# Optimization experiments

Measured on AMD Instinct MI355X. Metric: run time of the kernel, lower is better.

## Reference

```python
import jax, jax.numpy as jnp
import numpy as np
from jax import lax

V, E, H, B, P, Q = 50000, 300, 256, 32, 400, 40


def _cell(x, h, c, Wih, Whh, b):
    # torch nn.LSTMCell math (b = b_ih + b_hh), gate order i,f,g,o
    g = x @ Wih.T + h @ Whh.T + b
    i, f, gg, o = jnp.split(g, 4, axis=-1)
    c2 = jax.nn.sigmoid(f) * c + jax.nn.sigmoid(i) * jnp.tanh(gg)
    return jax.nn.sigmoid(o) * jnp.tanh(c2), c2


def setup_inputs():
    key = jax.random.key(0)
    ks = jax.random.split(key, 26)
    n = lambda k, s: jax.random.normal(k, s, jnp.float32) * 0.05
    return {
        "passage_ids": jax.random.randint(ks[0], (P, B), 0, V),
        "question_ids": jax.random.randint(ks[1], (Q, B), 0, V),
        "passage_lens": jax.random.randint(ks[2], (B,), P // 2, P + 1),
        "question_lens": jax.random.randint(ks[3], (B,), Q // 2, Q + 1),
        "answer": jax.random.randint(ks[4], (2, B), 0, P // 2),
        "embed": n(ks[5], (V, E)),
        "pre_Wih": n(ks[6], (4 * H, E)),
        "pre_Whh": n(ks[7], (4 * H, H)),
        "pre_b": n(ks[8], (4 * H,)),
        "Wq": n(ks[9], (H, H)),
        "Wp": n(ks[10], (H, H)),
        "bp": n(ks[11], (H,)),
        "Wh": n(ks[12], (H, H)),
        "w_alpha": n(ks[13], (H,)),
        "b_alpha": n(ks[14], ()),
        "m_Wih": n(ks[15], (4 * H, 2 * H)),
        "m_Whh": n(ks[16], (4 * H, H)),
        "m_b": n(ks[17], (4 * H,)),
        "Wm": n(ks[18], (2 * H, H)),
        "Wa": n(ks[19], (H, H)),
        "ba": n(ks[20], (H,)),
        "w_beta": n(ks[21], (H,)),
        "b_beta": n(ks[22], ()),
        "p_Wih": n(ks[23], (4 * H, 2 * H)),
        "p_Whh": n(ks[24], (4 * H, H)),
        "p_b": n(ks[25], (4 * H,)),
    }


def _forward(embed, pre_Wih, pre_Whh, pre_b, Wq, Wp, bp, Wh, w_alpha, b_alpha,
             m_Wih, m_Whh, m_b, Wm, Wa, ba, w_beta, b_beta, p_Wih, p_Whh, p_b,
             passage_ids, passage_lens, question_ids, question_lens):
    Hd = pre_Whh.shape[1]
    Bd = passage_ids.shape[1]
    z0 = jnp.zeros((Bd, Hd), jnp.float32)

    def preprocess(ids, lens):
        x = embed[ids]                                       # [T,B,E]
        T = x.shape[0]
        m = (jnp.arange(T)[:, None] < lens[None, :]).astype(jnp.float32)[:, :, None]  # [T,B,1]
        def step(carry, inp):
            h, c = carry
            xt, mt = inp
            _, c2 = _cell(xt, h, c, pre_Wih, pre_Whh, pre_b)
            h2 = jnp.tanh(c2) * mt                           # module quirk: h := tanh(c)
            return (h2, c2 * mt), h2
        _, Hs = lax.scan(step, (z0, z0), (x, m))
        return Hs, m

    Hp, mP = preprocess(passage_ids, passage_lens)           # [P,B,H]
    Hq, _ = preprocess(question_ids, question_lens)          # [Q,B,H]

    attQ = Hq @ Wq                                           # [Q,B,H]

    def match(Hp_dir, m_dir):
        def step(carry, inp):
            h, c = carry
            hp, mt = inp                                     # hp [B,H], mt [B,1]
            g = jnp.tanh(attQ + hp @ Wp + bp + h @ Wh)       # [Q,B,H]
            alpha = jax.nn.softmax(g @ w_alpha + b_alpha, axis=0)  # softmax over question time [Q,B]
            wq = jnp.einsum('qb,qbh->bh', alpha, Hq)
            zt = jnp.concatenate([hp, wq], axis=-1) * mt
            h2, c2 = _cell(zt, h, c, m_Wih, m_Whh, m_b)
            h2 = h2 * mt
            return (h2, c2 * mt), h2
        _, Hs = lax.scan(step, (z0, z0), (Hp_dir, m_dir))
        return Hs

    Hf = match(Hp, mP)
    Hb = match(Hp[::-1], mP[::-1])[::-1]
    Hr = jnp.concatenate([Hf, Hb], axis=-1)                  # [P,B,2H]

    attM = Hr @ Wm                                           # [P,B,H]
    valid = (jnp.arange(Hr.shape[0])[:, None] < passage_lens[None, :]).astype(jnp.float32)  # [P,B]
    ha, ca = z0, z0
    dists = []
    for _ in range(2):                                       # start / end pointer
        Fk = jnp.tanh(attM + ha @ Wa + ba)                   # [P,B,H]
        scores = Fk @ w_beta + b_beta                        # [P,B]
        scores = jnp.where(valid > 0, scores, -1e30)
        beta = jax.nn.softmax(scores, axis=0) * valid        # zeros past passage length, like original
        dists.append(beta.T)                                 # [B,P]
        wHr = jnp.einsum('pb,pbh->bh', beta, Hr)
        ha, ca = _cell(wHr, ha, ca, p_Wih, p_Whh, p_b)
    return jnp.stack(dists)                                  # [2,B,P]


def reference(passage_ids, question_ids, passage_lens, question_lens, answer,
              embed, pre_Wih, pre_Whh, pre_b, Wq, Wp, bp, Wh, w_alpha, b_alpha,
              m_Wih, m_Whh, m_b, Wm, Wa, ba, w_beta, b_beta, p_Wih, p_Whh, p_b):
    # `answer` only feeds the training loss in the original; forward returns the distributions.
    return _forward(embed, pre_Wih, pre_Whh, pre_b, Wq, Wp, bp, Wh, w_alpha, b_alpha,
                    m_Wih, m_Whh, m_b, Wm, Wa, ba, w_beta, b_beta, p_Wih, p_Whh, p_b,
                    passage_ids, passage_lens, question_ids, question_lens)
```

## Files before the change

### kernel.cpp

```cpp
#include <hip/hip_runtime.h>
#include <hip/hip_bf16.h>

typedef __attribute__((ext_vector_type(8))) short short8;
typedef __attribute__((ext_vector_type(4))) float f32x4;
typedef __attribute__((ext_vector_type(2))) float f32x2;
typedef unsigned short u16;
typedef unsigned int u32;

#define DEV __device__ __forceinline__

static constexpr int Hd    = 256;
static constexpr int Bb    = 32;
static constexpr int Pp    = 400;
static constexpr int Qq    = 40;
static constexpr int NROWS = Pp * Bb + Qq * Bb;
static constexpr int PROBE_MAGIC = 1234567;
static constexpr int NPROBE = 14;

DEV float bf2f(u16 u) { u32 i = ((u32)u) << 16; float f; __builtin_memcpy(&f, &i, 4); return f; }
DEV u16 f2bf(float f) { u32 i; __builtin_memcpy(&i, &f, 4); i += 0x7FFFu + ((i >> 16) & 1u); return (u16)(i >> 16); }
DEV float sigf(float x) { return __builtin_amdgcn_rcpf(1.f + __expf(-x)); }
DEV float tanhf_(float x) {
  float ax = __builtin_fabsf(x);
  float t = __expf(2.f * ax);
  float r = 1.f - 2.f * __builtin_amdgcn_rcpf(t + 1.f);
  return x < 0.f ? -r : r;
}
DEV f32x4 mfma32(short8 a, short8 b, f32x4 c) {
  return __builtin_amdgcn_mfma_f32_16x16x32_bf16(a, b, c, 0, 0, 0);
}
DEV short8 zero8() { short8 z = {0,0,0,0,0,0,0,0}; return z; }

struct KArgs {
  const int *pids, *qids, *plen, *qlen;
  const float *embedF, *preWihF, *preWhhF, *preBF, *WqF, *WpF, *bpF, *WhF,
              *walphaF, *balphaF, *mWihF, *mWhhF, *mBF, *WmF, *WaF, *baF,
              *wbetaF, *bbetaF, *pWihF, *pWhhF, *pBF;
  int* bar;
  u16 *WqT, *WpT, *WmT, *WihP, *Xpad, *preX, *Hp, *Hq, *Hrb, *wq, *wHr, *haB,
      *attQb, *pWihB, *pWhhB, *mWxb, *WhTb, *xW;
  float *hpWp, *attM, *scores, *aWa, *gatesW;
  float* out;
};

DEV void probe_mark(int* bar, int idx) {
  if (blockIdx.x == 0 && threadIdx.x == 0)
    __hip_atomic_store(bar + 768 + idx, PROBE_MAGIC, __ATOMIC_RELEASE, __HIP_MEMORY_SCOPE_AGENT);
}

DEV void barn(int* base, int grp, int n, int gen) {
  __syncthreads();
  if (threadIdx.x == 0) {
    int* c = base + grp * 128;
    int* g = base + grp * 128 + 64;
    if (__hip_atomic_fetch_add(c, 1, __ATOMIC_ACQ_REL, __HIP_MEMORY_SCOPE_AGENT) == n - 1) {
      __hip_atomic_store(c, 0, __ATOMIC_RELAXED, __HIP_MEMORY_SCOPE_AGENT);
      __hip_atomic_store(g, gen, __ATOMIC_RELEASE, __HIP_MEMORY_SCOPE_AGENT);
    } else {
      while (__hip_atomic_load(g, __ATOMIC_RELAXED, __HIP_MEMORY_SCOPE_AGENT) < gen)
        __builtin_amdgcn_s_sleep(1);
      __builtin_amdgcn_fence(__ATOMIC_ACQUIRE, "agent");
    }
  }
  __syncthreads();
}

__global__ __launch_bounds__(256) void k_prep(KArgs A) {
  const int gtid = blockIdx.x * 256 + threadIdx.x;
  const int GS = 256 * 256;
  for (int idx = gtid; idx < 1024 * 160; idx += GS) {
    int row = idx / 160, cd = idx - row * 160;
    u32 v = 0;
    if (cd < 150) {
      f32x2 e2 = *(const f32x2*)(A.preWihF + (size_t)row * 300 + cd * 2);
      v = (u32)f2bf(e2[0]) | ((u32)f2bf(e2[1]) << 16);
    }
    *(u32*)(A.WihP + (size_t)row * 320 + cd * 2) = v;
  }
  for (int idx = gtid; idx < NROWS * 160; idx += GS) {
    int row = idx / 160, cd = idx - row * 160;
    int id = (row < Pp * Bb) ? A.pids[row] : A.qids[row - Pp * Bb];
    u32 v = 0;
    if (cd < 150) {
      f32x2 e2 = *(const f32x2*)(A.embedF + (size_t)id * 300 + cd * 2);
      v = (u32)f2bf(e2[0]) | ((u32)f2bf(e2[1]) << 16);
    }
    *(u32*)(A.Xpad + (size_t)row * 320 + cd * 2) = v;
  }
  for (int idx = gtid; idx < 65536; idx += GS) {
    int r = idx >> 8, c = idx & 255;
    A.WqT[idx]  = f2bf(A.WqF[c * 256 + r]);
    A.WpT[idx]  = f2bf(A.WpF[c * 256 + r]);
    A.WhTb[idx] = f2bf(A.WhF[c * 256 + r]);
  }
  for (int idx = gtid; idx < 131072; idx += GS) {
    int r = idx >> 9, c = idx & 511;
    A.WmT[idx] = f2bf(A.WmF[c * 256 + r]);
  }
  for (int idx = gtid; idx < 1024 * 256; idx += GS) {
    int n = idx >> 8, k = idx & 255;
    A.mWxb[idx] = f2bf(A.mWihF[(size_t)n * 512 + k]);
  }
  for (int idx = gtid; idx < 524288 + 262144; idx += GS) {
    if (idx < 524288) A.pWihB[idx] = f2bf(A.pWihF[idx]);
    else              A.pWhhB[idx - 524288] = f2bf(A.pWhhF[idx - 524288]);
  }
  if (gtid < 32 * 256) {
    A.aWa[gtid] = A.baF[gtid & 255];
    A.haB[gtid] = 0;
  }
  probe_mark(A.bar, 0);
}

struct GemmArgs { const u16* Ag; int lda; const u16* Bg; int ldb; int Mt64, Nt64, nk; float* Cf; u16* Cb; int ldc; int* bar; int probe; };

__global__ __launch_bounds__(512) void k_gemm(GemmArgs g) {
  const int tid = threadIdx.x, lane = tid & 63;
  const int r16 = lane & 15, kl = (lane >> 4) * 8;
  const int ntile = g.Mt64 * g.Nt64;
  const int stride = gridDim.x * 8;
  for (int tix = blockIdx.x * 8 + (tid >> 6); tix < ntile; tix += stride) {
    int m0 = (tix / g.Nt64) * 64, n0 = (tix % g.Nt64) * 64;
    f32x4 acc[4][4] = {};
    for (int kb = 0; kb < g.nk; ++kb) {
      int k0 = kb * 32 + kl;
      short8 a[4], b[4];
#pragma unroll
      for (int i = 0; i < 4; ++i) {
        a[i] = *(const short8*)(g.Ag + (size_t)(m0 + i * 16 + r16) * g.lda + k0);
        b[i] = *(const short8*)(g.Bg + (size_t)(n0 + i * 16 + r16) * g.ldb + k0);
      }
#pragma unroll
      for (int mi = 0; mi < 4; ++mi)
#pragma unroll
        for (int ni = 0; ni < 4; ++ni) acc[mi][ni] = mfma32(a[mi], b[ni], acc[mi][ni]);
    }
#pragma unroll
    for (int mi = 0; mi < 4; ++mi)
#pragma unroll
      for (int ni = 0; ni < 4; ++ni)
#pragma unroll
        for (int j = 0; j < 4; ++j) {
          int r = m0 + mi * 16 + (lane >> 4) * 4 + j, cc = n0 + ni * 16 + r16;
          if (g.Cf) g.Cf[(size_t)r * g.ldc + cc] = acc[mi][ni][j];
          else      g.Cb[(size_t)r * g.ldc + cc] = f2bf(acc[mi][ni][j]);
        }
  }
  probe_mark(g.bar, g.probe);
}

__global__ __launch_bounds__(512) void k_prescan(KArgs A) {
  __shared__ __align__(16) unsigned char sm[33280];
  float* PRE = (float*)(sm + 24576);
  float* CL  = (float*)(sm + 30720);
  float* PBL = (float*)(sm + 32768);
  const int blk = blockIdx.x;
  const int gi  = blk & 15;
  const int grp = blk >> 4;
  const int steps  = grp ? Qq : Pp;
  const int* lens  = grp ? A.qlen : A.plen;
  u16* Hs          = grp ? A.Hq : A.Hp;
  const int xoff   = grp ? Pp * Bb : 0;

  const int tid = threadIdx.x, lane = tid & 63, wv = tid >> 6;
  const int r16 = lane & 15, kl = (lane >> 4) * 8;
  const int h0 = gi * 16;

  for (int idx = tid; idx < 48 * 256; idx += 512) {
    int row = idx >> 8, k = idx & 255;
    int gate = (row >> 4) * 256 + h0 + (row & 15);
    int byte = row * 512 + ((2 * k) ^ ((row & 7) << 4));
    *(u16*)(sm + byte) = f2bf(A.preWhhF[(size_t)gate * 256 + k]);
  }
  for (int idx = tid; idx < 32 * 16; idx += 512) CL[idx] = 0.f;
  if (tid < 48) PBL[tid] = A.preBF[(tid >> 4) * 256 + h0 + (tid & 15)];
  __syncthreads();

  int gen = 0;
#pragma unroll 1
  for (int t = 0; t < steps; ++t) {
    if (wv < 6) {
      int mi = wv & 1, ni = wv >> 1;
      int chain = mi * 16 + r16;
      f32x4 acc = {0.f, 0.f, 0.f, 0.f};
#pragma unroll
      for (int kb = 0; kb < 8; ++kb) {
        int k0 = kb * 32 + kl;
        short8 a = zero8();
        if (t > 0) a = *(const short8*)(Hs + (size_t)((t - 1) * 32 + chain) * 256 + k0);
        int row = ni * 16 + r16;
        short8 b = *(const short8*)(sm + row * 512 + ((2 * k0) ^ ((row & 7) << 4)));
        acc = mfma32(a, b, acc);
      }
      int col = ni * 16 + r16;
#pragma unroll
      for (int j = 0; j < 4; ++j)
        PRE[(mi * 16 + (lane >> 4) * 4 + j) * 48 + col] = acc[j];
    }
    __syncthreads();
    {
      int chain = tid >> 4, hd = tid & 15;
      size_t xr = (size_t)(xoff + t * 32 + chain) * 1024;
      float ip = PRE[chain * 48 + hd]      + bf2f(A.preX[xr + h0 + hd])       + PBL[hd];
      float fp = PRE[chain * 48 + 16 + hd] + bf2f(A.preX[xr + 256 + h0 + hd]) + PBL[16 + hd];
      float gp = PRE[chain * 48 + 32 + hd] + bf2f(A.preX[xr + 512 + h0 + hd]) + PBL[32 + hd];
      float c2 = sigf(fp) * CL[chain * 16 + hd] + sigf(ip) * tanhf_(gp);
      float mt = (t < lens[chain]) ? 1.f : 0.f;
      float h2 = tanhf_(c2) * mt;
      c2 *= mt;
      CL[chain * 16 + hd] = c2;
      Hs[(size_t)(t * 32 + chain) * 256 + h0 + hd] = f2bf(h2);
    }
    barn(A.bar, grp, 16, ++gen);
  }
  probe_mark(A.bar, 2);
}

__global__ __launch_bounds__(512) void k_match(KArgs A) {
  __shared__ __align__(16) unsigned char sm[81920];
  float* PRE = (float*)(sm + 65536);
  float* CL  = (float*)(sm + 73728);
  float* EL  = (float*)(sm + 75776);
  float* SL  = (float*)(sm + 77824);
  float* AL  = (float*)(sm + 78336);
  float* BPL = (float*)(sm + 78848);
  float* WAL = (float*)(sm + 79872);
  float* MBL = (float*)(sm + 80896);

  const int blk = blockIdx.x;
  const int gi  = blk & 15;
  const int dir = blk >> 4;
  const int grp = 2 + dir;
  const int tid = threadIdx.x, lane = tid & 63, wv = tid >> 6;
  const int r16 = lane & 15, kl = (lane >> 4) * 8;
  const int h0 = gi * 16;

  for (int idx = tid; idx < 64 * 512; idx += 512) {
    int row = idx >> 9, k = idx & 511;
    int gate = (row >> 4) * 256 + h0 + (row & 15);
    float v = (k < 256) ? A.mWihF[(size_t)gate * 512 + 256 + k]
                        : A.mWhhF[(size_t)gate * 256 + (k - 256)];
    int byte = row * 1024 + ((2 * k) ^ ((row & 7) << 4));
    *(u16*)(sm + byte) = f2bf(v);
  }
  for (int idx = tid; idx < 32 * 16; idx += 512) CL[idx] = 0.f;
  if (tid < 256) { BPL[tid] = A.bpF[tid]; WAL[tid] = A.walphaF[tid]; }
  if (tid < 64) MBL[tid] = A.mBF[(tid >> 4) * 256 + h0 + (tid & 15)];
  __syncthreads();

  const float bAl = A.balphaF[0];
  int gen = 0;
#pragma unroll 1
  for (int t = 0; t < Pp; ++t) {
    int p  = dir ? (Pp - 1 - t) : t;
    int pp = dir ? (p + 1) : (p - 1);
    barn(A.bar, grp, 16, ++gen);

    if (t == 0) {
      EL[tid] = 0.f;
    } else {
      f32x4 acc0 = {0.f,0.f,0.f,0.f}, acc1 = {0.f,0.f,0.f,0.f};
#pragma unroll
      for (int kb = 0; kb < 8; ++kb) {
        int k0 = kb * 32 + kl;
        short8 a = zero8();
        if (r16 < 2)
          a = *(const short8*)(A.Hrb + (size_t)(pp * 32 + gi * 2 + r16) * 512 + dir * 256 + k0);
        short8 bA = *(const short8*)(A.WhTb + (size_t)(wv * 32 + r16) * 256 + k0);
        short8 bB = *(const short8*)(A.WhTb + (size_t)(wv * 32 + 16 + r16) * 256 + k0);
        acc0 = mfma32(a, bA, acc0);
        acc1 = mfma32(a, bB, acc1);
      }
      if ((lane >> 4) == 0) {
        EL[0 * 256 + wv * 32 + r16]      = acc0[0];
        EL[1 * 256 + wv * 32 + r16]      = acc0[1];
        EL[0 * 256 + wv * 32 + 16 + r16] = acc1[0];
        EL[1 * 256 + wv * 32 + 16 + r16] = acc1[1];
      }
    }
    __syncthreads();
    {
      int c = wv >> 2;
      int b = gi * 2 + c;
      float base[4];
#pragma unroll
      for (int j = 0; j < 4; ++j) {
        int h = lane + 64 * j;
        base[j] = A.hpWp[(size_t)(p * 32 + b) * 256 + h] + BPL[h] + EL[c * 256 + h];
      }
      int q4 = wv & 3;
#pragma unroll
      for (int i = 0; i < 10; ++i) {
        int q = q4 + 4 * i;
        float s = 0.f;
#pragma unroll
        for (int j = 0; j < 4; ++j) {
          int h = lane + 64 * j;
          s += WAL[h] * tanhf_(bf2f(A.attQb[(size_t)(q * 32 + b) * 256 + h]) + base[j]);
        }
#pragma unroll
        for (int off = 32; off; off >>= 1) s += __shfl_xor(s, off, 64);
        if (lane == 0) SL[c * 40 + q] = s;
      }
    }
    __syncthreads();
    if ((wv & 3) == 0) {
      int c = wv >> 2;
      float x = (lane < 40) ? (SL[c * 40 + lane] + bAl) : -3.4e38f;
      float m = x;
#pragma unroll
      for (int off = 32; off; off >>= 1) m = fmaxf(m, __shfl_xor(m, off, 64));
      float e = (lane < 40) ? __expf(x - m) : 0.f;
      float su = e;
#pragma unroll
      for (int off = 32; off; off >>= 1) su += __shfl_xor(su, off, 64);
      if (lane < 40) AL[c * 40 + lane] = e / su;
    }
    __syncthreads();
    {
      int c = tid >> 8, h = tid & 255;
      int b = gi * 2 + c;
      float acc = 0.f;
#pragma unroll 8
      for (int q = 0; q < 40; ++q) acc += AL[c * 40 + q] * bf2f(A.Hq[(size_t)(q * 32 + b) * 256 + h]);
      float mt = (p < A.plen[b]) ? 1.f : 0.f;
      A.wq[(size_t)(dir * 32 + b) * 256 + h] = f2bf(acc * mt);
    }
    barn(A.bar, grp, 16, ++gen);

    {
      int mi = wv >> 2, ni = wv & 3;
      int chain = mi * 16 + r16;
      f32x4 acc = {0.f, 0.f, 0.f, 0.f};
#pragma unroll
      for (int kb = 0; kb < 16; ++kb) {
        int k0 = kb * 32 + kl;
        short8 a;
        if (kb < 8) a = *(const short8*)(A.wq + (size_t)(dir * 32 + chain) * 256 + k0);
        else {
          if (t == 0) a = zero8();
          else        a = *(const short8*)(A.Hrb + (size_t)(pp * 32 + chain) * 512 + dir * 256 + (k0 - 256));
        }
        int row = ni * 16 + r16;
        short8 b = *(const short8*)(sm + row * 1024 + ((2 * k0) ^ ((row & 7) << 4)));
        acc = mfma32(a, b, acc);
      }
      int col = ni * 16 + r16;
#pragma unroll
      for (int j = 0; j < 4; ++j)
        PRE[(mi * 16 + (lane >> 4) * 4 + j) * 64 + col] = acc[j];
    }
    __syncthreads();
    {
      int chain = tid >> 4, hd = tid & 15;
      size_t xr = (size_t)(p * 32 + chain) * 1024 + h0 + hd;
      float ig = PRE[chain * 64 + hd]      + MBL[hd]      + bf2f(A.xW[xr]);
      float fg = PRE[chain * 64 + 16 + hd] + MBL[16 + hd] + bf2f(A.xW[xr + 256]);
      float gg = PRE[chain * 64 + 32 + hd] + MBL[32 + hd] + bf2f(A.xW[xr + 512]);
      float og = PRE[chain * 64 + 48 + hd] + MBL[48 + hd] + bf2f(A.xW[xr + 768]);
      float c2 = sigf(fg) * CL[chain * 16 + hd] + sigf(ig) * tanhf_(gg);
      float h2 = sigf(og) * tanhf_(c2);
      float mt = (p < A.plen[chain]) ? 1.f : 0.f;
      c2 *= mt; h2 *= mt;
      CL[chain * 16 + hd] = c2;
      A.Hrb[(size_t)(p * 32 + chain) * 512 + dir * 256 + h0 + hd] = f2bf(h2);
    }
  }
  probe_mark(A.bar, 6);
}

__global__ __launch_bounds__(512) void k_scores(KArgs A, int probe) {
  const int blk = blockIdx.x, tid = threadIdx.x, lane = tid & 63, wv = tid >> 6;
  for (int j = wv; j < 50; j += 8) {
    int id = blk * 50 + j;
    int p = id >> 5, b = id & 31;
    float s = 0.f;
#pragma unroll
    for (int jj = 0; jj < 4; ++jj) {
      int h = lane + 64 * jj;
      s += A.wbetaF[h] * tanhf_(A.attM[(size_t)(p * 32 + b) * 256 + h] + A.aWa[b * 256 + h]);
    }
#pragma unroll
    for (int off = 32; off; off >>= 1) s += __shfl_xor(s, off, 64);
    if (lane == 0)
      A.scores[p * 32 + b] = (p < A.plen[b]) ? (s + A.bbetaF[0]) : -1e30f;
  }
  probe_mark(A.bar, probe);
}

__global__ __launch_bounds__(512) void k_soft(KArgs A, int k, int probe) {
  __shared__ __align__(16) unsigned char sm[2048];
  float* BL = (float*)sm;
  float* RED = (float*)(sm + 1664);
  const int b = blockIdx.x, tid = threadIdx.x, lane = tid & 63, wv = tid >> 6;
  float x = (tid < 400) ? A.scores[tid * 32 + b] : -3.4e38f;
  float m = x;
#pragma unroll
  for (int off = 32; off; off >>= 1) m = fmaxf(m, __shfl_xor(m, off, 64));
  if (lane == 0) RED[wv] = m;
  __syncthreads();
  if (tid == 0) {
    float mm = RED[0];
#pragma unroll
    for (int i = 1; i < 8; ++i) mm = fmaxf(mm, RED[i]);
    RED[0] = mm;
  }
  __syncthreads();
  float M = RED[0];
  float e = (tid < 400) ? __expf(x - M) : 0.f;
  float su = e;
#pragma unroll
  for (int off = 32; off; off >>= 1) su += __shfl_xor(su, off, 64);
  if (lane == 0) RED[8 + wv] = su;
  __syncthreads();
  if (tid == 0) {
    float ss = 0.f;
#pragma unroll
    for (int i = 0; i < 8; ++i) ss += RED[8 + i];
    RED[8] = ss;
  }
  __syncthreads();
  float SUM = RED[8];
  if (tid < 400) {
    float beta = (e / SUM) * ((tid < A.plen[b]) ? 1.f : 0.f);
    A.out[(size_t)(k * 32 + b) * 400 + tid] = beta;
    BL[tid] = beta;
  }
  if (k == 0) {
    __syncthreads();
    float acc = 0.f;
#pragma unroll 4
    for (int p = 0; p < 400; ++p) acc += BL[p] * bf2f(A.Hrb[(size_t)(p * 32 + b) * 512 + tid]);
    A.wHr[b * 512 + tid] = f2bf(acc);
  }
  probe_mark(A.bar, probe);
}

__global__ __launch_bounds__(128) void k_pgates(KArgs A) {
  const int blk = blockIdx.x, tid = threadIdx.x, lane = tid & 63, wv = tid >> 6;
  const int r16 = lane & 15, kl = (lane >> 4) * 8;
  const int g0 = blk * 16;
  const int mi = wv, chain = mi * 16 + r16;
  f32x4 acc = {0.f, 0.f, 0.f, 0.f};
#pragma unroll
  for (int kb = 0; kb < 24; ++kb) {
    int k0 = kb * 32 + kl;
    short8 a, b;
    if (kb < 16) {
      a = *(const short8*)(A.wHr + (size_t)chain * 512 + k0);
      b = *(const short8*)(A.pWihB + (size_t)(g0 + r16) * 512 + k0);
    } else {
      a = *(const short8*)(A.haB + (size_t)chain * 256 + (k0 - 512));
      b = *(const short8*)(A.pWhhB + (size_t)(g0 + r16) * 256 + (k0 - 512));
    }
    acc = mfma32(a, b, acc);
  }
#pragma unroll
  for (int j = 0; j < 4; ++j)
    A.gatesW[(size_t)(mi * 16 + (lane >> 4) * 4 + j) * 1024 + g0 + r16] = acc[j];
  probe_mark(A.bar, 10);
}

__global__ __launch_bounds__(256) void k_pcell(KArgs A) {
  __shared__ float HL[256];
  const int b = blockIdx.x, hd = threadIdx.x;
  {
    float ig = A.gatesW[(size_t)b * 1024 + hd]       + A.pBF[hd];
    float gg = A.gatesW[(size_t)b * 1024 + 512 + hd] + A.pBF[512 + hd];
    float og = A.gatesW[(size_t)b * 1024 + 768 + hd] + A.pBF[768 + hd];
    float c2 = sigf(ig) * tanhf_(gg);
    float h2 = sigf(og) * tanhf_(c2);
    HL[hd] = h2;
    A.haB[b * 256 + hd] = f2bf(h2);
  }
  __syncthreads();
  {
    float acc = A.baF[hd];
#pragma unroll 8
    for (int kk = 0; kk < 256; ++kk) acc += HL[kk] * A.WaF[(size_t)kk * 256 + hd];
    A.aWa[b * 256 + hd] = acc;
  }
  probe_mark(A.bar, 11);
}

__global__ __launch_bounds__(64) void k_diag(KArgs A) {
  if (threadIdx.x == 0 && blockIdx.x == 0) {
    int bad = -1;
    for (int i = 0; i < NPROBE; ++i) {
      int v = __hip_atomic_load(A.bar + 768 + i, __ATOMIC_ACQUIRE, __HIP_MEMORY_SCOPE_AGENT);
      if (v != PROBE_MAGIC) { bad = i; break; }
    }
    if (bad >= 0) {
      float s = 128.f * (float)(1 << bad);
      for (int j = 0; j < 8; ++j) A.out[j] = s;
    }
  }
}

extern "C" void kernel_launch(void* const* d_in, const int* in_sizes, int n_in,
                              void* d_out, int out_size, void* d_ws, size_t ws_size,
                              hipStream_t stream) {
  (void)in_sizes; (void)n_in; (void)ws_size;
  KArgs A;
  A.pids = (const int*)d_in[0];
  A.qids = (const int*)d_in[1];
  A.plen = (const int*)d_in[2];
  A.qlen = (const int*)d_in[3];
  A.embedF  = (const float*)d_in[5];
  A.preWihF = (const float*)d_in[6];
  A.preWhhF = (const float*)d_in[7];
  A.preBF   = (const float*)d_in[8];
  A.WqF     = (const float*)d_in[9];
  A.WpF     = (const float*)d_in[10];
  A.bpF     = (const float*)d_in[11];
  A.WhF     = (const float*)d_in[12];
  A.walphaF = (const float*)d_in[13];
  A.balphaF = (const float*)d_in[14];
  A.mWihF   = (const float*)d_in[15];
  A.mWhhF   = (const float*)d_in[16];
  A.mBF     = (const float*)d_in[17];
  A.WmF     = (const float*)d_in[18];
  A.WaF     = (const float*)d_in[19];
  A.baF     = (const float*)d_in[20];
  A.wbetaF  = (const float*)d_in[21];
  A.bbetaF  = (const float*)d_in[22];
  A.pWihF   = (const float*)d_in[23];
  A.pWhhF   = (const float*)d_in[24];
  A.pBF     = (const float*)d_in[25];

  char* w = (char*)d_ws;
  size_t off = 0;
  auto take = [&](size_t bytes) { void* p = w + off; off += (bytes + 255) & ~(size_t)255; return p; };
  A.bar    = (int*)take(4096);
  A.WqT    = (u16*)take(256 * 256 * 2);
  A.WpT    = (u16*)take(256 * 256 * 2);
  A.WmT    = (u16*)take(256 * 512 * 2);
  A.WihP   = (u16*)take((size_t)1024 * 320 * 2);
  A.Xpad   = (u16*)take((size_t)NROWS * 320 * 2);
  A.preX   = (u16*)take((size_t)NROWS * 1024 * 2);
  A.Hp     = (u16*)take((size_t)Pp * Bb * 256 * 2);
  A.Hq     = (u16*)take((size_t)Qq * Bb * 256 * 2);
  A.Hrb    = (u16*)take((size_t)Pp * Bb * 512 * 2);
  A.wq     = (u16*)take(2 * 32 * 256 * 2);
  A.wHr    = (u16*)take(32 * 512 * 2);
  A.haB    = (u16*)take(32 * 256 * 2);
  A.attQb  = (u16*)take((size_t)Qq * Bb * 256 * 2);
  A.pWihB  = (u16*)take((size_t)1024 * 512 * 2);
  A.pWhhB  = (u16*)take((size_t)1024 * 256 * 2);
  A.mWxb   = (u16*)take((size_t)1024 * 256 * 2);
  A.WhTb   = (u16*)take((size_t)256 * 256 * 2);
  A.hpWp   = (float*)take((size_t)Pp * Bb * 256 * 4);
  A.attM   = (float*)take((size_t)Pp * Bb * 256 * 4);
  A.scores = (float*)take((size_t)Pp * Bb * 4);
  A.aWa    = (float*)take(32 * 256 * 4);
  A.gatesW = (float*)take((size_t)32 * 1024 * 4);
  A.xW     = A.preX;
  A.out    = (float*)d_out;

  hipMemsetAsync(d_out, 0x3C, 64, stream);
  hipMemsetAsync(A.bar, 0, 4096, stream);

  (void)hipGetLastError();
  size_t outB = (size_t)out_size * 4;
  int li = 0;
#define CK  if (hipGetLastError() != hipSuccess) { hipMemsetAsync(d_out, 0x41 + li, outB, stream); return; } ++li;

  hipLaunchKernelGGL(k_prep, dim3(256), dim3(256), 0, stream, A); CK;

  GemmArgs g1{A.Xpad, 320, A.WihP, 320, NROWS / 64, 16, 10, nullptr, A.preX, 1024, A.bar, 1};
  hipLaunchKernelGGL(k_gemm, dim3(256), dim3(512), 0, stream, g1); CK;

  hipLaunchKernelGGL(k_prescan, dim3(32), dim3(512), 0, stream, A); CK;

  GemmArgs g2{A.Hq, 256, A.WqT, 256, 20, 4, 8, nullptr, A.attQb, 256, A.bar, 3};
  hipLaunchKernelGGL(k_gemm, dim3(16), dim3(512), 0, stream, g2); CK;
  GemmArgs g3{A.Hp, 256, A.WpT, 256, 200, 4, 8, A.hpWp, nullptr, 256, A.bar, 4};
  hipLaunchKernelGGL(k_gemm, dim3(128), dim3(512), 0, stream, g3); CK;
  GemmArgs gx{A.Hp, 256, A.mWxb, 256, 200, 16, 8, nullptr, A.xW, 1024, A.bar, 5};
  hipLaunchKernelGGL(k_gemm, dim3(256), dim3(512), 0, stream, gx); CK;

  hipLaunchKernelGGL(k_match, dim3(32), dim3(512), 0, stream, A); CK;

  GemmArgs g4{A.Hrb, 512, A.WmT, 512, 200, 4, 16, A.attM, nullptr, 256, A.bar, 7};
  hipLaunchKernelGGL(k_gemm, dim3(128), dim3(512), 0, stream, g4); CK;

  hipLaunchKernelGGL(k_scores, dim3(256), dim3(512), 0, stream, A, 8); CK;
  hipLaunchKernelGGL(k_soft,   dim3(32),  dim3(512), 0, stream, A, 0, 9); CK;
  hipLaunchKernelGGL(k_pgates, dim3(64),  dim3(128), 0, stream, A); CK;
  hipLaunchKernelGGL(k_pcell,  dim3(32),  dim3(256), 0, stream, A); CK;
  hipLaunchKernelGGL(k_scores, dim3(256), dim3(512), 0, stream, A, 12); CK;
  hipLaunchKernelGGL(k_soft,   dim3(32),  dim3(512), 0, stream, A, 1, 13); CK;

  hipLaunchKernelGGL(k_diag,   dim3(1),   dim3(64),  0, stream, A); CK;
#undef CK
}
```

Measured before the change: 9.596 ms.

## Repartition recurrent LSTM scans by batch chains to drop grid barriers

The prescan and match recurrent kernels used to split the hidden dimension across 16 blocks per sequence, which needed a global atomic barrier every timestep. Each block now owns 4 whole batch chains and all hidden units, so a step needs only __syncthreads, and the hidden/attention state stays in LDS instead of round-tripping through global memory. The trade-off is that each block streams the full recurrent weight matrices from global/L2 every step instead of a cached LDS slice, and the MFMA tiles are mostly padding (4 of 16 rows used). Weights are pre-converted to bf16 in k_prep, and the unused barrier helper and wq buffer are removed.

```diff
diff --git a/kernel.cpp b/kernel.cpp
--- a/kernel.cpp
+++ b/kernel.cpp
@@ -37,8 +37,8 @@
               *walphaF, *balphaF, *mWihF, *mWhhF, *mBF, *WmF, *WaF, *baF,
               *wbetaF, *bbetaF, *pWihF, *pWhhF, *pBF;
   int* bar;
-  u16 *WqT, *WpT, *WmT, *WihP, *Xpad, *preX, *Hp, *Hq, *Hrb, *wq, *wHr, *haB,
-      *attQb, *pWihB, *pWhhB, *mWxb, *WhTb, *xW;
+  u16 *WqT, *WpT, *WmT, *WihP, *Xpad, *preX, *Hp, *Hq, *Hrb, *wHr, *haB,
+      *attQb, *pWihB, *pWhhB, *mWxb, *WhTb, *preWhhB, *mWgb, *xW;
   float *hpWp, *attM, *scores, *aWa, *gatesW;
   float* out;
 };
@@ -46,23 +46,6 @@
 DEV void probe_mark(int* bar, int idx) {
   if (blockIdx.x == 0 && threadIdx.x == 0)
     __hip_atomic_store(bar + 768 + idx, PROBE_MAGIC, __ATOMIC_RELEASE, __HIP_MEMORY_SCOPE_AGENT);
-}
-
-DEV void barn(int* base, int grp, int n, int gen) {
-  __syncthreads();
-  if (threadIdx.x == 0) {
-    int* c = base + grp * 128;
-    int* g = base + grp * 128 + 64;
-    if (__hip_atomic_fetch_add(c, 1, __ATOMIC_ACQ_REL, __HIP_MEMORY_SCOPE_AGENT) == n - 1) {
-      __hip_atomic_store(c, 0, __ATOMIC_RELAXED, __HIP_MEMORY_SCOPE_AGENT);
-      __hip_atomic_store(g, gen, __ATOMIC_RELEASE, __HIP_MEMORY_SCOPE_AGENT);
-    } else {
-      while (__hip_atomic_load(g, __ATOMIC_RELAXED, __HIP_MEMORY_SCOPE_AGENT) < gen)
-        __builtin_amdgcn_s_sleep(1);
-      __builtin_amdgcn_fence(__ATOMIC_ACQUIRE, "agent");
-    }
-  }
-  __syncthreads();
 }
 
 __global__ __launch_bounds__(256) void k_prep(KArgs A) {
@@ -100,6 +83,14 @@
   for (int idx = gtid; idx < 1024 * 256; idx += GS) {
     int n = idx >> 8, k = idx & 255;
     A.mWxb[idx] = f2bf(A.mWihF[(size_t)n * 512 + k]);
+  }
+  for (int idx = gtid; idx < 768 * 256; idx += GS)
+    A.preWhhB[idx] = f2bf(A.preWhhF[idx]);
+  for (int idx = gtid; idx < 1024 * 512; idx += GS) {
+    int n = idx >> 9, k = idx & 511;
+    float v = (k < 256) ? A.mWihF[(size_t)n * 512 + 256 + k]
+                        : A.mWhhF[(size_t)n * 256 + (k - 256)];
+    A.mWgb[idx] = f2bf(v);
   }
   for (int idx = gtid; idx < 524288 + 262144; idx += GS) {
     if (idx < 524288) A.pWihB[idx] = f2bf(A.pWihF[idx]);
@@ -150,163 +141,152 @@
 }
 
 __global__ __launch_bounds__(512) void k_prescan(KArgs A) {
-  __shared__ __align__(16) unsigned char sm[33280];
-  float* PRE = (float*)(sm + 24576);
-  float* CL  = (float*)(sm + 30720);
-  float* PBL = (float*)(sm + 32768);
+  __shared__ __align__(16) unsigned char sm[22528];
+  u16*   HF  = (u16*)sm;
+  float* CS  = (float*)(sm + 2048);
+  float* PRE = (float*)(sm + 6144);
+  float* PBL = (float*)(sm + 18432);
   const int blk = blockIdx.x;
-  const int gi  = blk & 15;
-  const int grp = blk >> 4;
-  const int steps  = grp ? Qq : Pp;
-  const int* lens  = grp ? A.qlen : A.plen;
-  u16* Hs          = grp ? A.Hq : A.Hp;
-  const int xoff   = grp ? Pp * Bb : 0;
-
+  const int isQ = blk >> 3;
+  const int c0  = (blk & 7) * 4;
+  const int steps = isQ ? Qq : Pp;
+  const int* lens = isQ ? A.qlen : A.plen;
+  u16* Hs = isQ ? A.Hq : A.Hp;
+  const int xoff = isQ ? Pp * Bb : 0;
   const int tid = threadIdx.x, lane = tid & 63, wv = tid >> 6;
   const int r16 = lane & 15, kl = (lane >> 4) * 8;
-  const int h0 = gi * 16;
-
-  for (int idx = tid; idx < 48 * 256; idx += 512) {
-    int row = idx >> 8, k = idx & 255;
-    int gate = (row >> 4) * 256 + h0 + (row & 15);
-    int byte = row * 512 + ((2 * k) ^ ((row & 7) << 4));
-    *(u16*)(sm + byte) = f2bf(A.preWhhF[(size_t)gate * 256 + k]);
-  }
-  for (int idx = tid; idx < 32 * 16; idx += 512) CL[idx] = 0.f;
-  if (tid < 48) PBL[tid] = A.preBF[(tid >> 4) * 256 + h0 + (tid & 15)];
-  __syncthreads();
-
-  int gen = 0;
+
+  for (int idx = tid; idx < 768; idx += 512) PBL[idx] = A.preBF[idx];
+  for (int idx = tid; idx < 4 * 256; idx += 512) { CS[idx] = 0.f; HF[idx] = 0; }
+  __syncthreads();
+
+  const int cC = tid >> 7, hh = (tid & 127) * 2;
+  const int bC = c0 + cC;
+  const int lenC = lens[bC];
+
 #pragma unroll 1
   for (int t = 0; t < steps; ++t) {
-    if (wv < 6) {
-      int mi = wv & 1, ni = wv >> 1;
-      int chain = mi * 16 + r16;
+#pragma unroll
+    for (int i = 0; i < 6; ++i) {
+      int n = wv + 8 * i;
       f32x4 acc = {0.f, 0.f, 0.f, 0.f};
 #pragma unroll
       for (int kb = 0; kb < 8; ++kb) {
         int k0 = kb * 32 + kl;
-        short8 a = zero8();
-        if (t > 0) a = *(const short8*)(Hs + (size_t)((t - 1) * 32 + chain) * 256 + k0);
-        int row = ni * 16 + r16;
-        short8 b = *(const short8*)(sm + row * 512 + ((2 * k0) ^ ((row & 7) << 4)));
+        short8 a = (r16 < 4) ? *(const short8*)(HF + r16 * 256 + k0) : zero8();
+        short8 b = *(const short8*)(A.preWhhB + (size_t)(n * 16 + r16) * 256 + k0);
         acc = mfma32(a, b, acc);
       }
-      int col = ni * 16 + r16;
-#pragma unroll
-      for (int j = 0; j < 4; ++j)
-        PRE[(mi * 16 + (lane >> 4) * 4 + j) * 48 + col] = acc[j];
+      if ((lane >> 4) == 0) {
+#pragma unroll
+        for (int j = 0; j < 4; ++j) PRE[j * 768 + n * 16 + r16] = acc[j];
+      }
     }
     __syncthreads();
     {
-      int chain = tid >> 4, hd = tid & 15;
-      size_t xr = (size_t)(xoff + t * 32 + chain) * 1024;
-      float ip = PRE[chain * 48 + hd]      + bf2f(A.preX[xr + h0 + hd])       + PBL[hd];
-      float fp = PRE[chain * 48 + 16 + hd] + bf2f(A.preX[xr + 256 + h0 + hd]) + PBL[16 + hd];
-      float gp = PRE[chain * 48 + 32 + hd] + bf2f(A.preX[xr + 512 + h0 + hd]) + PBL[32 + hd];
-      float c2 = sigf(fp) * CL[chain * 16 + hd] + sigf(ip) * tanhf_(gp);
-      float mt = (t < lens[chain]) ? 1.f : 0.f;
-      float h2 = tanhf_(c2) * mt;
-      c2 *= mt;
-      CL[chain * 16 + hd] = c2;
-      Hs[(size_t)(t * 32 + chain) * 256 + h0 + hd] = f2bf(h2);
-    }
-    barn(A.bar, grp, 16, ++gen);
+      size_t xr = (size_t)(xoff + t * 32 + bC) * 1024;
+      u32 x0 = *(const u32*)(A.preX + xr + hh);
+      u32 x1 = *(const u32*)(A.preX + xr + 256 + hh);
+      u32 x2 = *(const u32*)(A.preX + xr + 512 + hh);
+      u16 hb[2];
+#pragma unroll
+      for (int u = 0; u < 2; ++u) {
+        int h = hh + u;
+        float xi = bf2f(u ? (u16)(x0 >> 16) : (u16)x0);
+        float xf = bf2f(u ? (u16)(x1 >> 16) : (u16)x1);
+        float xg = bf2f(u ? (u16)(x2 >> 16) : (u16)x2);
+        float ip = PRE[cC * 768 + h]       + xi + PBL[h];
+        float fp = PRE[cC * 768 + 256 + h] + xf + PBL[256 + h];
+        float gp = PRE[cC * 768 + 512 + h] + xg + PBL[512 + h];
+        float c2 = sigf(fp) * CS[cC * 256 + h] + sigf(ip) * tanhf_(gp);
+        float mt = (t < lenC) ? 1.f : 0.f;
+        float h2 = tanhf_(c2) * mt;
+        CS[cC * 256 + h] = c2 * mt;
+        hb[u] = f2bf(h2);
+      }
+      u32 pk = (u32)hb[0] | ((u32)hb[1] << 16);
+      *(u32*)(HF + cC * 256 + hh) = pk;
+      *(u32*)(Hs + (size_t)(t * 32 + bC) * 256 + hh) = pk;
+    }
+    __syncthreads();
   }
   probe_mark(A.bar, 2);
 }
 
 __global__ __launch_bounds__(512) void k_match(KArgs A) {
-  __shared__ __align__(16) unsigned char sm[81920];
-  float* PRE = (float*)(sm + 65536);
-  float* CL  = (float*)(sm + 73728);
-  float* EL  = (float*)(sm + 75776);
-  float* SL  = (float*)(sm + 77824);
-  float* AL  = (float*)(sm + 78336);
-  float* BPL = (float*)(sm + 78848);
-  float* WAL = (float*)(sm + 79872);
-  float* MBL = (float*)(sm + 80896);
+  __shared__ __align__(16) unsigned char sm[36864];
+  u16*   AF  = (u16*)sm;
+  float* CS  = (float*)(sm + 4096);
+  float* E   = (float*)(sm + 8192);
+  float* PRE = (float*)(sm + 12288);
+  float* SL  = (float*)(sm + 28672);
+  float* AL  = (float*)(sm + 29440);
+  float* BPL = (float*)(sm + 30208);
+  float* WAL = (float*)(sm + 31232);
+  float* MBL = (float*)(sm + 32256);
 
   const int blk = blockIdx.x;
-  const int gi  = blk & 15;
-  const int dir = blk >> 4;
-  const int grp = 2 + dir;
+  const int dir = blk >> 3;
+  const int c0  = (blk & 7) * 4;
   const int tid = threadIdx.x, lane = tid & 63, wv = tid >> 6;
   const int r16 = lane & 15, kl = (lane >> 4) * 8;
-  const int h0 = gi * 16;
-
-  for (int idx = tid; idx < 64 * 512; idx += 512) {
-    int row = idx >> 9, k = idx & 511;
-    int gate = (row >> 4) * 256 + h0 + (row & 15);
-    float v = (k < 256) ? A.mWihF[(size_t)gate * 512 + 256 + k]
-                        : A.mWhhF[(size_t)gate * 256 + (k - 256)];
-    int byte = row * 1024 + ((2 * k) ^ ((row & 7) << 4));
-    *(u16*)(sm + byte) = f2bf(v);
-  }
-  for (int idx = tid; idx < 32 * 16; idx += 512) CL[idx] = 0.f;
+
+  for (int idx = tid; idx < 4 * 512; idx += 512) AF[idx] = 0;
+  for (int idx = tid; idx < 4 * 256; idx += 512) CS[idx] = 0.f;
   if (tid < 256) { BPL[tid] = A.bpF[tid]; WAL[tid] = A.walphaF[tid]; }
-  if (tid < 64) MBL[tid] = A.mBF[(tid >> 4) * 256 + h0 + (tid & 15)];
+  for (int idx = tid; idx < 1024; idx += 512) MBL[idx] = A.mBF[idx];
   __syncthreads();
 
   const float bAl = A.balphaF[0];
-  int gen = 0;
+  const int cA = wv >> 1, qh = wv & 1, bA = c0 + cA;
+  const int cC = tid >> 7, hh = (tid & 127) * 2, bC = c0 + cC;
+  const int lenC = A.plen[bC];
+
 #pragma unroll 1
   for (int t = 0; t < Pp; ++t) {
-    int p  = dir ? (Pp - 1 - t) : t;
-    int pp = dir ? (p + 1) : (p - 1);
-    barn(A.bar, grp, 16, ++gen);
-
-    if (t == 0) {
-      EL[tid] = 0.f;
-    } else {
-      f32x4 acc0 = {0.f,0.f,0.f,0.f}, acc1 = {0.f,0.f,0.f,0.f};
+    int p = dir ? (Pp - 1 - t) : t;
+
+#pragma unroll
+    for (int i = 0; i < 2; ++i) {
+      int n = wv * 2 + i;
+      f32x4 acc = {0.f, 0.f, 0.f, 0.f};
 #pragma unroll
       for (int kb = 0; kb < 8; ++kb) {
         int k0 = kb * 32 + kl;
-        short8 a = zero8();
-        if (r16 < 2)
-          a = *(const short8*)(A.Hrb + (size_t)(pp * 32 + gi * 2 + r16) * 512 + dir * 256 + k0);
-        short8 bA = *(const short8*)(A.WhTb + (size_t)(wv * 32 + r16) * 256 + k0);
-        short8 bB = *(const short8*)(A.WhTb + (size_t)(wv * 32 + 16 + r16) * 256 + k0);
-        acc0 = mfma32(a, bA, acc0);
-        acc1 = mfma32(a, bB, acc1);
+        short8 a = (r16 < 4) ? *(const short8*)(AF + r16 * 512 + 256 + k0) : zero8();
+        short8 b = *(const short8*)(A.WhTb + (size_t)(n * 16 + r16) * 256 + k0);
+        acc = mfma32(a, b, acc);
       }
       if ((lane >> 4) == 0) {
-        EL[0 * 256 + wv * 32 + r16]      = acc0[0];
-        EL[1 * 256 + wv * 32 + r16]      = acc0[1];
-        EL[0 * 256 + wv * 32 + 16 + r16] = acc1[0];
-        EL[1 * 256 + wv * 32 + 16 + r16] = acc1[1];
+#pragma unroll
+        for (int j = 0; j < 4; ++j) E[j * 256 + n * 16 + r16] = acc[j];
       }
     }
     __syncthreads();
     {
-      int c = wv >> 2;
-      int b = gi * 2 + c;
       float base[4];
 #pragma unroll
       for (int j = 0; j < 4; ++j) {
         int h = lane + 64 * j;
-        base[j] = A.hpWp[(size_t)(p * 32 + b) * 256 + h] + BPL[h] + EL[c * 256 + h];
-      }
-      int q4 = wv & 3;
-#pragma unroll
-      for (int i = 0; i < 10; ++i) {
-        int q = q4 + 4 * i;
+        base[j] = A.hpWp[(size_t)(p * 32 + bA) * 256 + h] + BPL[h] + E[cA * 256 + h];
+      }
+#pragma unroll
+      for (int i = 0; i < 20; ++i) {
+        int q = qh * 20 + i;
         float s = 0.f;
 #pragma unroll
         for (int j = 0; j < 4; ++j) {
           int h = lane + 64 * j;
-          s += WAL[h] * tanhf_(bf2f(A.attQb[(size_t)(q * 32 + b) * 256 + h]) + base[j]);
+          s += WAL[h] * tanhf_(bf2f(A.attQb[(size_t)(q * 32 + bA) * 256 + h]) + base[j]);
         }
 #pragma unroll
         for (int off = 32; off; off >>= 1) s += __shfl_xor(s, off, 64);
-        if (lane == 0) SL[c * 40 + q] = s;
-      }
-    }
-    __syncthreads();
-    if ((wv & 3) == 0) {
-      int c = wv >> 2;
-      float x = (lane < 40) ? (SL[c * 40 + lane] + bAl) : -3.4e38f;
+        if (lane == 0) SL[cA * 40 + q] = s;
+      }
+    }
+    __syncthreads();
+    if (wv < 4) {
+      float x = (lane < 40) ? (SL[wv * 40 + lane] + bAl) : -3.4e38f;
       float m = x;
 #pragma unroll
       for (int off = 32; off; off >>= 1) m = fmaxf(m, __shfl_xor(m, off, 64));
@@ -314,57 +294,64 @@
       float su = e;
 #pragma unroll
       for (int off = 32; off; off >>= 1) su += __shfl_xor(su, off, 64);
-      if (lane < 40) AL[c * 40 + lane] = e / su;
+      if (lane < 40) AL[wv * 40 + lane] = e / su;
     }
     __syncthreads();
     {
-      int c = tid >> 8, h = tid & 255;
-      int b = gi * 2 + c;
-      float acc = 0.f;
+      float a0 = 0.f, a1 = 0.f;
 #pragma unroll 8
-      for (int q = 0; q < 40; ++q) acc += AL[c * 40 + q] * bf2f(A.Hq[(size_t)(q * 32 + b) * 256 + h]);
-      float mt = (p < A.plen[b]) ? 1.f : 0.f;
-      A.wq[(size_t)(dir * 32 + b) * 256 + h] = f2bf(acc * mt);
-    }
-    barn(A.bar, grp, 16, ++gen);
-
-    {
-      int mi = wv >> 2, ni = wv & 3;
-      int chain = mi * 16 + r16;
+      for (int q = 0; q < 40; ++q) {
+        u32 w = *(const u32*)(A.Hq + (size_t)(q * 32 + bC) * 256 + hh);
+        float al = AL[cC * 40 + q];
+        a0 += al * bf2f((u16)w);
+        a1 += al * bf2f((u16)(w >> 16));
+      }
+      float mt = (p < lenC) ? 1.f : 0.f;
+      *(u32*)(AF + cC * 512 + hh) = (u32)f2bf(a0 * mt) | ((u32)f2bf(a1 * mt) << 16);
+    }
+    __syncthreads();
+#pragma unroll
+    for (int i = 0; i < 8; ++i) {
+      int n = wv + 8 * i;
       f32x4 acc = {0.f, 0.f, 0.f, 0.f};
 #pragma unroll
       for (int kb = 0; kb < 16; ++kb) {
         int k0 = kb * 32 + kl;
-        short8 a;
-        if (kb < 8) a = *(const short8*)(A.wq + (size_t)(dir * 32 + chain) * 256 + k0);
-        else {
-          if (t == 0) a = zero8();
-          else        a = *(const short8*)(A.Hrb + (size_t)(pp * 32 + chain) * 512 + dir * 256 + (k0 - 256));
-        }
-        int row = ni * 16 + r16;
-        short8 b = *(const short8*)(sm + row * 1024 + ((2 * k0) ^ ((row & 7) << 4)));
+        short8 a = (r16 < 4) ? *(const short8*)(AF + r16 * 512 + k0) : zero8();
+        short8 b = *(const short8*)(A.mWgb + (size_t)(n * 16 + r16) * 512 + k0);
         acc = mfma32(a, b, acc);
       }
-      int col = ni * 16 + r16;
-#pragma unroll
-      for (int j = 0; j < 4; ++j)
-        PRE[(mi * 16 + (lane >> 4) * 4 + j) * 64 + col] = acc[j];
+      if ((lane >> 4) == 0) {
+#pragma unroll
+        for (int j = 0; j < 4; ++j) PRE[j * 1024 + n * 16 + r16] = acc[j];
+      }
     }
     __syncthreads();
     {
-      int chain = tid >> 4, hd = tid & 15;
-      size_t xr = (size_t)(p * 32 + chain) * 1024 + h0 + hd;
-      float ig = PRE[chain * 64 + hd]      + MBL[hd]      + bf2f(A.xW[xr]);
-      float fg = PRE[chain * 64 + 16 + hd] + MBL[16 + hd] + bf2f(A.xW[xr + 256]);
-      float gg = PRE[chain * 64 + 32 + hd] + MBL[32 + hd] + bf2f(A.xW[xr + 512]);
-      float og = PRE[chain * 64 + 48 + hd] + MBL[48 + hd] + bf2f(A.xW[xr + 768]);
-      float c2 = sigf(fg) * CL[chain * 16 + hd] + sigf(ig) * tanhf_(gg);
-      float h2 = sigf(og) * tanhf_(c2);
-      float mt = (p < A.plen[chain]) ? 1.f : 0.f;
-      c2 *= mt; h2 *= mt;
-      CL[chain * 16 + hd] = c2;
-      A.Hrb[(size_t)(p * 32 + chain) * 512 + dir * 256 + h0 + hd] = f2bf(h2);
-    }
+      size_t xr = (size_t)(p * 32 + bC) * 1024;
+      u32 x0 = *(const u32*)(A.xW + xr + hh);
+      u32 x1 = *(const u32*)(A.xW + xr + 256 + hh);
+      u32 x2 = *(const u32*)(A.xW + xr + 512 + hh);
+      u32 x3 = *(const u32*)(A.xW + xr + 768 + hh);
+      u16 hb[2];
+#pragma unroll
+      for (int u = 0; u < 2; ++u) {
+        int h = hh + u;
+        float ig = PRE[cC * 1024 + h]       + MBL[h]       + bf2f(u ? (u16)(x0 >> 16) : (u16)x0);
+        float fg = PRE[cC * 1024 + 256 + h] + MBL[256 + h] + bf2f(u ? (u16)(x1 >> 16) : (u16)x1);
+        float gg = PRE[cC * 1024 + 512 + h] + MBL[512 + h] + bf2f(u ? (u16)(x2 >> 16) : (u16)x2);
+        float og = PRE[cC * 1024 + 768 + h] + MBL[768 + h] + bf2f(u ? (u16)(x3 >> 16) : (u16)x3);
+        float c2 = sigf(fg) * CS[cC * 256 + h] + sigf(ig) * tanhf_(gg);
+        float h2 = sigf(og) * tanhf_(c2);
+        float mt = (p < lenC) ? 1.f : 0.f;
+        CS[cC * 256 + h] = c2 * mt;
+        hb[u] = f2bf(h2 * mt);
+      }
+      u32 pk = (u32)hb[0] | ((u32)hb[1] << 16);
+      *(u32*)(AF + cC * 512 + 256 + hh) = pk;
+      *(u32*)(A.Hrb + (size_t)(p * 32 + bC) * 512 + dir * 256 + hh) = pk;
+    }
+    __syncthreads();
   }
   probe_mark(A.bar, 6);
 }
@@ -531,31 +518,32 @@
   char* w = (char*)d_ws;
   size_t off = 0;
   auto take = [&](size_t bytes) { void* p = w + off; off += (bytes + 255) & ~(size_t)255; return p; };
-  A.bar    = (int*)take(4096);
-  A.WqT    = (u16*)take(256 * 256 * 2);
-  A.WpT    = (u16*)take(256 * 256 * 2);
-  A.WmT    = (u16*)take(256 * 512 * 2);
-  A.WihP   = (u16*)take((size_t)1024 * 320 * 2);
-  A.Xpad   = (u16*)take((size_t)NROWS * 320 * 2);
-  A.preX   = (u16*)take((size_t)NROWS * 1024 * 2);
-  A.Hp     = (u16*)take((size_t)Pp * Bb * 256 * 2);
-  A.Hq     = (u16*)take((size_t)Qq * Bb * 256 * 2);
-  A.Hrb    = (u16*)take((size_t)Pp * Bb * 512 * 2);
-  A.wq     = (u16*)take(2 * 32 * 256 * 2);
-  A.wHr    = (u16*)take(32 * 512 * 2);
-  A.haB    = (u16*)take(32 * 256 * 2);
-  A.attQb  = (u16*)take((size_t)Qq * Bb * 256 * 2);
-  A.pWihB  = (u16*)take((size_t)1024 * 512 * 2);
-  A.pWhhB  = (u16*)take((size_t)1024 * 256 * 2);
-  A.mWxb   = (u16*)take((size_t)1024 * 256 * 2);
-  A.WhTb   = (u16*)take((size_t)256 * 256 * 2);
-  A.hpWp   = (float*)take((size_t)Pp * Bb * 256 * 4);
-  A.attM   = (float*)take((size_t)Pp * Bb * 256 * 4);
-  A.scores = (float*)take((size_t)Pp * Bb * 4);
-  A.aWa    = (float*)take(32 * 256 * 4);
-  A.gatesW = (float*)take((size_t)32 * 1024 * 4);
-  A.xW     = A.preX;
-  A.out    = (float*)d_out;
+  A.bar     = (int*)take(4096);
+  A.WqT     = (u16*)take(256 * 256 * 2);
+  A.WpT     = (u16*)take(256 * 256 * 2);
+  A.WmT     = (u16*)take(256 * 512 * 2);
+  A.WihP    = (u16*)take((size_t)1024 * 320 * 2);
+  A.Xpad    = (u16*)take((size_t)NROWS * 320 * 2);
+  A.preX    = (u16*)take((size_t)NROWS * 1024 * 2);
+  A.Hp      = (u16*)take((size_t)Pp * Bb * 256 * 2);
+  A.Hq      = (u16*)take((size_t)Qq * Bb * 256 * 2);
+  A.Hrb     = (u16*)take((size_t)Pp * Bb * 512 * 2);
+  A.wHr     = (u16*)take(32 * 512 * 2);
+  A.haB     = (u16*)take(32 * 256 * 2);
+  A.attQb   = (u16*)take((size_t)Qq * Bb * 256 * 2);
+  A.pWihB   = (u16*)take((size_t)1024 * 512 * 2);
+  A.pWhhB   = (u16*)take((size_t)1024 * 256 * 2);
+  A.mWxb    = (u16*)take((size_t)1024 * 256 * 2);
+  A.WhTb    = (u16*)take((size_t)256 * 256 * 2);
+  A.preWhhB = (u16*)take((size_t)768 * 256 * 2);
+  A.mWgb    = (u16*)take((size_t)1024 * 512 * 2);
+  A.hpWp    = (float*)take((size_t)Pp * Bb * 256 * 4);
+  A.attM    = (float*)take((size_t)Pp * Bb * 256 * 4);
+  A.scores  = (float*)take((size_t)Pp * Bb * 4);
+  A.aWa     = (float*)take(32 * 256 * 4);
+  A.gatesW  = (float*)take((size_t)32 * 1024 * 4);
+  A.xW      = A.preX;
+  A.out     = (float*)d_out;
 
   hipMemsetAsync(d_out, 0x3C, 64, stream);
   hipMemsetAsync(A.bar, 0, 4096, stream);
@@ -570,7 +558,7 @@
   GemmArgs g1{A.Xpad, 320, A.WihP, 320, NROWS / 64, 16, 10, nullptr, A.preX, 1024, A.bar, 1};
   hipLaunchKernelGGL(k_gemm, dim3(256), dim3(512), 0, stream, g1); CK;
 
-  hipLaunchKernelGGL(k_prescan, dim3(32), dim3(512), 0, stream, A); CK;
+  hipLaunchKernelGGL(k_prescan, dim3(16), dim3(512), 0, stream, A); CK;
 
   GemmArgs g2{A.Hq, 256, A.WqT, 256, 20, 4, 8, nullptr, A.attQb, 256, A.bar, 3};
   hipLaunchKernelGGL(k_gemm, dim3(16), dim3(512), 0, stream, g2); CK;
@@ -579,7 +567,7 @@
   GemmArgs gx{A.Hp, 256, A.mWxb, 256, 200, 16, 8, nullptr, A.xW, 1024, A.bar, 5};
   hipLaunchKernelGGL(k_gemm, dim3(256), dim3(512), 0, stream, gx); CK;
 
-  hipLaunchKernelGGL(k_match, dim3(32), dim3(512), 0, stream, A); CK;
+  hipLaunchKernelGGL(k_match, dim3(16), dim3(512), 0, stream, A); CK;
 
   GemmArgs g4{A.Hrb, 512, A.WmT, 512, 200, 4, 16, A.attM, nullptr, 256, A.bar, 7};
   hipLaunchKernelGGL(k_gemm, dim3(128), dim3(512), 0, stream, g4); CK;
```

New measurement: 21.36 ms. 123% more time.
